# Performance work log

Hardware: AMD Instinct MI355X
Metric: run time of the kernel (lower is better)

The kernel has to match this reference:

```python
import jax, jax.numpy as jnp
import numpy as np

B, N_SRC, N_TGT = 2, 2048, 2048
DIM, HEADS, DIM_HEAD, DIM_ROT = 1024, 16, 64, 32
INNER = HEADS * DIM_HEAD
SCALE = DIM_HEAD ** -0.5


def rotate_every_two(x):
    # (..., d) with d even: pairs (x1, x2) -> (-x2, x1), interleaved
    x1 = x[..., ::2]
    x2 = x[..., 1::2]
    return jnp.stack((-x2, x1), axis=-1).reshape(x.shape)


def setup_inputs() -> dict:
    key = jax.random.key(0)
    ks = jax.random.split(key, 10)
    return {
        "src": jax.random.normal(ks[0], (B, N_SRC, DIM), jnp.float32),
        "sin_src": jax.random.uniform(ks[1], (B, N_SRC, DIM_ROT), jnp.float32, -1.0, 1.0),
        "cos_src": jax.random.uniform(ks[2], (B, N_SRC, DIM_ROT), jnp.float32, -1.0, 1.0),
        "tgt": jax.random.normal(ks[3], (B, N_TGT, DIM), jnp.float32),
        "sin_tgt": jax.random.uniform(ks[4], (B, N_TGT, DIM_ROT), jnp.float32, -1.0, 1.0),
        "cos_tgt": jax.random.uniform(ks[5], (B, N_TGT, DIM_ROT), jnp.float32, -1.0, 1.0),
        "wq": jax.random.normal(ks[6], (DIM, INNER), jnp.float32) / np.sqrt(DIM),
        "wkv": jax.random.normal(ks[7], (DIM, 2 * INNER), jnp.float32) / np.sqrt(DIM),
        "wout": jax.random.normal(ks[8], (INNER, DIM), jnp.float32) / np.sqrt(INNER),
        "bout": jnp.zeros((DIM,), jnp.float32),
    }


def reference(src, sin_src, cos_src, tgt, sin_tgt, cos_tgt, wq, wkv, wout, bout):
    b = src.shape[0]
    q = tgt @ wq                                  # (b, i, inner)
    k, v = jnp.split(src @ wkv, 2, axis=-1)       # (b, j, inner) each

    def split_heads(t):
        return t.reshape(b, t.shape[1], HEADS, DIM_HEAD).transpose(0, 2, 1, 3)

    q, k, v = map(split_heads, (q, k, v))          # (b, h, n, d)

    # rotary on leading DIM_ROT dims; pos embs broadcast across heads
    st, ct = sin_tgt[:, None], cos_tgt[:, None]    # (b, 1, i, dr)
    ss, cs = sin_src[:, None], cos_src[:, None]    # (b, 1, j, dr)
    q_rot, q_pass = q[..., :DIM_ROT], q[..., DIM_ROT:]
    k_rot, k_pass = k[..., :DIM_ROT], k[..., DIM_ROT:]
    q_rot = q_rot * ct + rotate_every_two(q_rot) * st
    k_rot = k_rot * cs + rotate_every_two(k_rot) * ss
    q = jnp.concatenate([q_rot, q_pass], axis=-1)
    k = jnp.concatenate([k_rot, k_pass], axis=-1)

    dots = jnp.einsum('bhid,bhjd->bhij', q, k) * SCALE
    attn = jax.nn.softmax(dots, axis=-1)
    out = jnp.einsum('bhij,bhjd->bhid', attn, v)
    out = out.transpose(0, 2, 1, 3).reshape(b, out.shape[2], INNER)
    return out @ wout + bout, attn
```

## Files before the change

kernel.cpp:

```cpp
#include <hip/hip_runtime.h>
#include <hip/hip_bf16.h>
#include <cstdint>
#include <cstddef>

#define NB 2
#define NSEQ 2048
#define NHEADS 16
#define HD 64
#define DMODEL 1024
#define SCALEF 0.125f

typedef __attribute__((ext_vector_type(4))) float f32x4;
typedef __attribute__((ext_vector_type(8))) short s16x8;

__device__ __forceinline__ unsigned short f2bf(float f) {
  union { float f; unsigned u; } v; v.f = f;
  unsigned u = v.u;
  return (unsigned short)((u + 0x7fffu + ((u >> 16) & 1u)) >> 16);
}
__device__ __forceinline__ float bf2f(unsigned short s) {
  union { unsigned u; float f; } v; v.u = ((unsigned)s) << 16;
  return v.f;
}

__global__ void k_convert2(const float* __restrict__ a, const float* __restrict__ b,
                           unsigned short* __restrict__ oa, unsigned short* __restrict__ ob) {
  int bx = blockIdx.x;
  const float* in = (bx < 4096) ? a : b;
  unsigned short* out = (bx < 4096) ? oa : ob;
  int i = (bx & 4095) * 256 + threadIdx.x;
  float4 v = ((const float4*)in)[i];
  ushort4 o;
  o.x = f2bf(v.x); o.y = f2bf(v.y); o.z = f2bf(v.z); o.w = f2bf(v.w);
  ((ushort4*)out)[i] = o;
}

__global__ void k_transpose_all(const float* __restrict__ wq, unsigned short* __restrict__ wq_t,
                                const float* __restrict__ wkv, unsigned short* __restrict__ wkv_t,
                                const float* __restrict__ wout, unsigned short* __restrict__ wout_t) {
  const int z = blockIdx.z;
  const float* w; unsigned short* wt; int N;
  if (z == 0)      { w = wq;   wt = wq_t;   N = 1024; }
  else if (z == 1) { w = wkv;  wt = wkv_t;  N = 2048; }
  else             { w = wout; wt = wout_t; N = 1024; }
  if (blockIdx.x * 64 >= N) return;
  __shared__ float t[64][65];
  int n0 = blockIdx.x * 64, k0 = blockIdx.y * 64;
  int c = threadIdx.x & 63, rb = threadIdx.x >> 6;
#pragma unroll
  for (int rr = 0; rr < 16; rr++) {
    int k = rb * 16 + rr;
    t[c][k] = w[(size_t)(k0 + k) * N + n0 + c];
  }
  __syncthreads();
#pragma unroll
  for (int rr = 0; rr < 16; rr++) {
    int n = rb * 16 + rr;
    wt[(size_t)(n0 + n) * 1024 + k0 + c] = f2bf(t[n][c]);
  }
}

#define GLD16(gp, lp) __builtin_amdgcn_global_load_lds( \
    (const __attribute__((address_space(1))) unsigned int*)(gp), \
    (__attribute__((address_space(3))) unsigned int*)(lp), 16, 0, 0)

#define GEMM_BODY(A, Bt)                                                        \
  __shared__ unsigned short As[128 * 32];                                       \
  __shared__ unsigned short Bs[128 * 32];                                       \
  const int tid = threadIdx.x;                                                  \
  const int lane = tid & 63, wid = tid >> 6;                                    \
  const int m0 = blockIdx.y * 128, n0 = blockIdx.x * 128;                       \
  const int wr = wid >> 1, wc = wid & 1;                                        \
  const int lr = lane >> 2, l4 = lane & 3;                                      \
  const int lc = lane & 15, lg = lane >> 4;                                     \
  const unsigned short* pa0 = A + (size_t)(m0 + wid * 32 + lr) * 1024 + l4 * 8; \
  const unsigned short* pa1 = pa0 + (size_t)16 * 1024;                          \
  const unsigned short* pb0 = Bt + (size_t)(n0 + wid * 32 + lr) * 1024 + l4 * 8;\
  const unsigned short* pb1 = pb0 + (size_t)16 * 1024;                          \
  f32x4 acc[4][4] = {};                                                         \
  for (int kt = 0; kt < 1024; kt += 32) {                                       \
    GLD16(pa0 + kt, &As[wid * 1024]);                                           \
    GLD16(pa1 + kt, &As[wid * 1024 + 512]);                                     \
    GLD16(pb0 + kt, &Bs[wid * 1024]);                                           \
    GLD16(pb1 + kt, &Bs[wid * 1024 + 512]);                                     \
    __syncthreads();                                                            \
    s16x8 af[4], bfr[4];                                                        \
    _Pragma("unroll")                                                           \
    for (int m = 0; m < 4; m++)                                                 \
      af[m] = *(const s16x8*)&As[(wr * 64 + m * 16 + lc) * 32 + lg * 8];        \
    _Pragma("unroll")                                                           \
    for (int n = 0; n < 4; n++)                                                 \
      bfr[n] = *(const s16x8*)&Bs[(wc * 64 + n * 16 + lc) * 32 + lg * 8];       \
    __builtin_amdgcn_s_setprio(1);                                              \
    _Pragma("unroll")                                                           \
    for (int m = 0; m < 4; m++)                                                 \
      _Pragma("unroll")                                                         \
      for (int n = 0; n < 4; n++)                                               \
        acc[m][n] = __builtin_amdgcn_mfma_f32_16x16x32_bf16(af[m], bfr[n], acc[m][n], 0, 0, 0); \
    __builtin_amdgcn_s_setprio(0);                                              \
    __syncthreads();                                                            \
  }

__global__ __launch_bounds__(256) void k_gemm(const unsigned short* __restrict__ A,
                                              const unsigned short* __restrict__ Bt,
                                              float* __restrict__ C,
                                              const float* __restrict__ bias) {
  GEMM_BODY(A, Bt)
  float bv[4];
#pragma unroll
  for (int n = 0; n < 4; n++) bv[n] = bias[n0 + wc * 64 + n * 16 + lc];
#pragma unroll
  for (int m = 0; m < 4; m++) {
#pragma unroll
    for (int n = 0; n < 4; n++) {
      int col = n0 + wc * 64 + n * 16 + lc;
#pragma unroll
      for (int r = 0; r < 4; r++) {
        int row = m0 + wr * 64 + m * 16 + lg * 4 + r;
        C[(size_t)row * 1024 + col] = acc[m][n][r] + bv[n];
      }
    }
  }
}

__global__ __launch_bounds__(256) void k_gemmq(const unsigned short* __restrict__ A,
                                               const unsigned short* __restrict__ Bt,
                                               const float* __restrict__ sinp,
                                               const float* __restrict__ cosp,
                                               unsigned short* __restrict__ qhb) {
  GEMM_BODY(A, Bt)
#pragma unroll
  for (int m = 0; m < 4; m++) {
#pragma unroll
    for (int n = 0; n < 4; n++) {
      int c = n0 + wc * 64 + n * 16 + lc;
      int h = c >> 6, d = c & 63;
      bool dorope = (d < 32);
#pragma unroll
      for (int r = 0; r < 4; r++) {
        int row = m0 + wr * 64 + m * 16 + lg * 4 + r;
        float x = acc[m][n][r];
        float px = __shfl_xor(x, 1);
        float o = x;
        if (dorope) {
          float s = sinp[(size_t)row * 32 + d];
          float cz = cosp[(size_t)row * 32 + d];
          o = (d & 1) ? (x * cz + px * s) : (x * cz - px * s);
        }
        int b = row >> 11, i = row & 2047;
        qhb[((size_t)(b * NHEADS + h) * NSEQ + i) * HD + d] = f2bf(o);
      }
    }
  }
}

__global__ __launch_bounds__(256) void k_gemmkv(const unsigned short* __restrict__ A,
                                                const unsigned short* __restrict__ Bt,
                                                const float* __restrict__ sinp,
                                                const float* __restrict__ cosp,
                                                unsigned short* __restrict__ khb,
                                                unsigned short* __restrict__ vtb) {
  GEMM_BODY(A, Bt)
#pragma unroll
  for (int m = 0; m < 4; m++) {
#pragma unroll
    for (int n = 0; n < 4; n++) {
      int c = n0 + wc * 64 + n * 16 + lc;
      int d = c & 63;
      if (c < 1024) {
        int h = c >> 6;
        bool dorope = (d < 32);
#pragma unroll
        for (int r = 0; r < 4; r++) {
          int row = m0 + wr * 64 + m * 16 + lg * 4 + r;
          float x = acc[m][n][r];
          float px = __shfl_xor(x, 1);
          float o = x;
          if (dorope) {
            float s = sinp[(size_t)row * 32 + d];
            float cz = cosp[(size_t)row * 32 + d];
            o = (d & 1) ? (x * cz + px * s) : (x * cz - px * s);
          }
          int b = row >> 11, i = row & 2047;
          khb[((size_t)(b * NHEADS + h) * NSEQ + i) * HD + d] = f2bf(o);
        }
      } else {
        int h = (c - 1024) >> 6;
#pragma unroll
        for (int r = 0; r < 4; r++) (void)__shfl_xor(acc[m][n][r], 1);
        ushort4 o;
        o.x = f2bf(acc[m][n][0]); o.y = f2bf(acc[m][n][1]);
        o.z = f2bf(acc[m][n][2]); o.w = f2bf(acc[m][n][3]);
        int row0 = m0 + wr * 64 + m * 16 + lg * 4;
        int b = row0 >> 11, i = row0 & 2047;
        *(ushort4*)&vtb[((size_t)(b * NHEADS + h) * HD + d) * NSEQ + i] = o;
      }
    }
  }
}

#define QBLK 32
#define SROWB 2056
__global__ __launch_bounds__(1024, 4) void k_attn(const unsigned short* __restrict__ qh,
                                                  const unsigned short* __restrict__ kh,
                                                  const unsigned short* __restrict__ vt,
                                                  float* __restrict__ attn_g,
                                                  unsigned short* __restrict__ ctx) {
  __shared__ unsigned short Sbf[QBLK * SROWB];
  __shared__ float wred[16][32];
  __shared__ float invr[32];
  float* part = (float*)Sbf;

  const int tid = threadIdx.x;
  const int lane = tid & 63, wid = tid >> 6;
  const int bid = blockIdx.x;
  const int g = bid & 31, t = bid >> 5;
  const int h = g & 15, b = g >> 4;
  const int i0 = t * QBLK;
  const int lc = lane & 15, lg = lane >> 4;
  const int wcb = wid * 128;

  const unsigned short* qb = qh + ((size_t)(b * NHEADS + h) * NSEQ + i0) * HD;
  const unsigned short* kb = kh + (size_t)(b * NHEADS + h) * NSEQ * HD;
  const unsigned short* vb = vt + (size_t)(b * NHEADS + h) * HD * NSEQ;

  s16x8 aq[2][2];
#pragma unroll
  for (int rg = 0; rg < 2; rg++) {
    aq[rg][0] = *(const s16x8*)&qb[(rg * 16 + lc) * HD + lg * 8];
    aq[rg][1] = *(const s16x8*)&qb[(rg * 16 + lc) * HD + 32 + lg * 8];
  }
  float psum[2][4] = {};
  const unsigned short* krow = kb + (size_t)(wcb + lc) * HD + lg * 8;
  s16x8 kp[2][2];
  kp[0][0] = *(const s16x8*)&krow[0];
  kp[0][1] = *(const s16x8*)&krow[32];
#pragma unroll
  for (int jf = 0; jf < 8; jf++) {
    if (jf < 7) {
      kp[(jf + 1) & 1][0] = *(const s16x8*)&krow[(size_t)((jf + 1) * 16) * HD];
      kp[(jf + 1) & 1][1] = *(const s16x8*)&krow[(size_t)((jf + 1) * 16) * HD + 32];
    }
    int j = wcb + jf * 16;
#pragma unroll
    for (int rg = 0; rg < 2; rg++) {
      f32x4 acc = {};
      acc = __builtin_amdgcn_mfma_f32_16x16x32_bf16(aq[rg][0], kp[jf & 1][0], acc, 0, 0, 0);
      acc = __builtin_amdgcn_mfma_f32_16x16x32_bf16(aq[rg][1], kp[jf & 1][1], acc, 0, 0, 0);
#pragma unroll
      for (int r = 0; r < 4; r++) {
        float e = __expf(acc[r] * SCALEF);
        psum[rg][r] += e;
        Sbf[(size_t)(rg * 16 + lg * 4 + r) * SROWB + j + lc] = f2bf(e);
      }
    }
  }
#pragma unroll
  for (int off = 1; off <= 8; off <<= 1)
#pragma unroll
    for (int rg = 0; rg < 2; rg++)
#pragma unroll
      for (int r = 0; r < 4; r++) psum[rg][r] += __shfl_xor(psum[rg][r], off);
  if (lc == 0) {
#pragma unroll
    for (int rg = 0; rg < 2; rg++)
#pragma unroll
      for (int r = 0; r < 4; r++) wred[wid][rg * 16 + lg * 4 + r] = psum[rg][r];
  }
  __syncthreads();
  if (tid < 32) {
    float tot = 0.f;
#pragma unroll
    for (int w = 0; w < 16; w++) tot += wred[w][tid];
    invr[tid] = 1.0f / tot;
  }
  __syncthreads();

  const int srow = tid >> 5;
  const int scc = (tid & 31) * 8;
  const float sinv = invr[srow];
  float* arow = attn_g + ((size_t)(b * NHEADS + h) * NSEQ + i0 + srow) * NSEQ + scc;

  f32x4 accd[2][4] = {};
  const unsigned short* vrow = vb + (size_t)lc * NSEQ + wcb + lg * 8;
  s16x8 vp[2][4];
#pragma unroll
  for (int f = 0; f < 4; f++)
    vp[0][f] = *(const s16x8*)&vrow[(size_t)(f * 16) * NSEQ];
#pragma unroll
  for (int jj = 0; jj < 4; jj++) {
    if (jj < 3) {
#pragma unroll
      for (int f = 0; f < 4; f++)
        vp[(jj + 1) & 1][f] = *(const s16x8*)&vrow[(size_t)(f * 16) * NSEQ + (jj + 1) * 32];
    }
    int jb = wcb + jj * 32;
    s16x8 af0 = *(const s16x8*)&Sbf[(size_t)lc * SROWB + jb + lg * 8];
    __builtin_amdgcn_s_setprio(1);
#pragma unroll
    for (int f = 0; f < 4; f++)
      accd[0][f] = __builtin_amdgcn_mfma_f32_16x16x32_bf16(af0, vp[jj & 1][f], accd[0][f], 0, 0, 0);
    __builtin_amdgcn_s_setprio(0);
    s16x8 af1 = *(const s16x8*)&Sbf[(size_t)(16 + lc) * SROWB + jb + lg * 8];
    __builtin_amdgcn_s_setprio(1);
#pragma unroll
    for (int f = 0; f < 4; f++)
      accd[1][f] = __builtin_amdgcn_mfma_f32_16x16x32_bf16(af1, vp[jj & 1][f], accd[1][f], 0, 0, 0);
    __builtin_amdgcn_s_setprio(0);
#pragma unroll
    for (int kk = 0; kk < 2; kk++) {
      int k = jj * 2 + kk;
      s16x8 ev = *(const s16x8*)&Sbf[(size_t)srow * SROWB + scc + k * 256];
      f32x4 f0, f1;
      f0[0] = bf2f((unsigned short)ev[0]) * sinv;
      f0[1] = bf2f((unsigned short)ev[1]) * sinv;
      f0[2] = bf2f((unsigned short)ev[2]) * sinv;
      f0[3] = bf2f((unsigned short)ev[3]) * sinv;
      f1[0] = bf2f((unsigned short)ev[4]) * sinv;
      f1[1] = bf2f((unsigned short)ev[5]) * sinv;
      f1[2] = bf2f((unsigned short)ev[6]) * sinv;
      f1[3] = bf2f((unsigned short)ev[7]) * sinv;
      *(f32x4*)&arow[k * 256] = f0;
      *(f32x4*)&arow[k * 256 + 4] = f1;
    }
  }
  __syncthreads();

  if (wid < 8) {
#pragma unroll
    for (int rg = 0; rg < 2; rg++)
#pragma unroll
      for (int f = 0; f < 4; f++)
#pragma unroll
        for (int r = 0; r < 4; r++)
          part[((size_t)wid * 32 + rg * 16 + lg * 4 + r) * 65 + f * 16 + lc] = accd[rg][f][r];
  }
  __syncthreads();
  if (wid >= 8) {
#pragma unroll
    for (int rg = 0; rg < 2; rg++)
#pragma unroll
      for (int f = 0; f < 4; f++)
#pragma unroll
        for (int r = 0; r < 4; r++)
          part[((size_t)(wid - 8) * 32 + rg * 16 + lg * 4 + r) * 65 + f * 16 + lc] += accd[rg][f][r];
  }
  __syncthreads();

  {
    const int oi = tid >> 5;
    const int d0 = (tid & 31) * 2;
    float s0 = 0.f, s1 = 0.f;
#pragma unroll
    for (int p = 0; p < 8; p++) {
      s0 += part[((size_t)p * 32 + oi) * 65 + d0];
      s1 += part[((size_t)p * 32 + oi) * 65 + d0 + 1];
    }
    float iv = invr[oi];
    ushort2 o;
    o.x = f2bf(s0 * iv);
    o.y = f2bf(s1 * iv);
    *(ushort2*)&ctx[(size_t)(b * NSEQ + i0 + oi) * DMODEL + h * HD + d0] = o;
  }
}

extern "C" void kernel_launch(void* const* d_in, const int* in_sizes, int n_in,
                              void* d_out, int out_size, void* d_ws, size_t ws_size,
                              hipStream_t stream) {
  const float* src     = (const float*)d_in[0];
  const float* sin_src = (const float*)d_in[1];
  const float* cos_src = (const float*)d_in[2];
  const float* tgt     = (const float*)d_in[3];
  const float* sin_tgt = (const float*)d_in[4];
  const float* cos_tgt = (const float*)d_in[5];
  const float* wq      = (const float*)d_in[6];
  const float* wkv     = (const float*)d_in[7];
  const float* wout    = (const float*)d_in[8];
  const float* bout    = (const float*)d_in[9];

  if (ws_size < (size_t)109051904) return;

  uint8_t* w = (uint8_t*)d_ws;
  unsigned short* tgt_bf = (unsigned short*)(w + 0);
  unsigned short* src_bf = (unsigned short*)(w + 8388608);
  unsigned short* wq_t   = (unsigned short*)(w + 16777216);
  unsigned short* wkv_t  = (unsigned short*)(w + 18874368);
  unsigned short* wout_t = (unsigned short*)(w + 23068672);
  unsigned short* qhb    = (unsigned short*)(w + 75497472);
  unsigned short* khb    = (unsigned short*)(w + 83886080);
  unsigned short* vtb    = (unsigned short*)(w + 92274688);
  unsigned short* ctx    = (unsigned short*)(w + 100663296);

  float* out_p  = (float*)d_out;
  float* attn_p = out_p + (size_t)NB * NSEQ * DMODEL;

  k_convert2<<<8192, 256, 0, stream>>>(tgt, src, tgt_bf, src_bf);
  k_transpose_all<<<dim3(32, 16, 3), 256, 0, stream>>>(wq, wq_t, wkv, wkv_t, wout, wout_t);

  k_gemmq <<<dim3(8, 32),  256, 0, stream>>>(tgt_bf, wq_t,  sin_tgt, cos_tgt, qhb);
  k_gemmkv<<<dim3(16, 32), 256, 0, stream>>>(src_bf, wkv_t, sin_src, cos_src, khb, vtb);

  k_attn<<<2048, 1024, 0, stream>>>(qhb, khb, vtb, attn_p, ctx);

  k_gemm<<<dim3(8, 32), 256, 0, stream>>>(ctx, wout_t, out_p, bout);
}
```

Before: 337.8 us.

## Halve attention query block to 16 rows with 512-thread blocks

The attention kernel now processes 16 query rows per block with 8 waves, each covering 256 keys, instead of 32 rows with 16 waves covering 128 keys. Grid doubles to 4096 blocks and LDS per block halves, which lets more blocks reside per CU and shortens each block's serial phases. In exchange, every K/V element is reloaded twice as often across blocks, and each wave now runs longer loops with fewer MFMAs per loaded K/V fragment.

```diff
diff --git a/kernel.cpp b/kernel.cpp
--- a/kernel.cpp
+++ b/kernel.cpp
@@ -199,16 +199,16 @@
   }
 }
 
-#define QBLK 32
+#define QBLK 16
 #define SROWB 2056
-__global__ __launch_bounds__(1024, 4) void k_attn(const unsigned short* __restrict__ qh,
-                                                  const unsigned short* __restrict__ kh,
-                                                  const unsigned short* __restrict__ vt,
-                                                  float* __restrict__ attn_g,
-                                                  unsigned short* __restrict__ ctx) {
+__global__ __launch_bounds__(512, 4) void k_attn(const unsigned short* __restrict__ qh,
+                                                 const unsigned short* __restrict__ kh,
+                                                 const unsigned short* __restrict__ vt,
+                                                 float* __restrict__ attn_g,
+                                                 unsigned short* __restrict__ ctx) {
   __shared__ unsigned short Sbf[QBLK * SROWB];
-  __shared__ float wred[16][32];
-  __shared__ float invr[32];
+  __shared__ float wred[8][16];
+  __shared__ float invr[16];
   float* part = (float*)Sbf;
 
   const int tid = threadIdx.x;
@@ -218,60 +218,49 @@
   const int h = g & 15, b = g >> 4;
   const int i0 = t * QBLK;
   const int lc = lane & 15, lg = lane >> 4;
-  const int wcb = wid * 128;
+  const int wcb = wid * 256;
 
   const unsigned short* qb = qh + ((size_t)(b * NHEADS + h) * NSEQ + i0) * HD;
   const unsigned short* kb = kh + (size_t)(b * NHEADS + h) * NSEQ * HD;
   const unsigned short* vb = vt + (size_t)(b * NHEADS + h) * HD * NSEQ;
 
-  s16x8 aq[2][2];
-#pragma unroll
-  for (int rg = 0; rg < 2; rg++) {
-    aq[rg][0] = *(const s16x8*)&qb[(rg * 16 + lc) * HD + lg * 8];
-    aq[rg][1] = *(const s16x8*)&qb[(rg * 16 + lc) * HD + 32 + lg * 8];
-  }
-  float psum[2][4] = {};
+  s16x8 aq0 = *(const s16x8*)&qb[lc * HD + lg * 8];
+  s16x8 aq1 = *(const s16x8*)&qb[lc * HD + 32 + lg * 8];
+  float psum[4] = {};
   const unsigned short* krow = kb + (size_t)(wcb + lc) * HD + lg * 8;
   s16x8 kp[2][2];
   kp[0][0] = *(const s16x8*)&krow[0];
   kp[0][1] = *(const s16x8*)&krow[32];
 #pragma unroll
-  for (int jf = 0; jf < 8; jf++) {
-    if (jf < 7) {
+  for (int jf = 0; jf < 16; jf++) {
+    if (jf < 15) {
       kp[(jf + 1) & 1][0] = *(const s16x8*)&krow[(size_t)((jf + 1) * 16) * HD];
       kp[(jf + 1) & 1][1] = *(const s16x8*)&krow[(size_t)((jf + 1) * 16) * HD + 32];
     }
     int j = wcb + jf * 16;
-#pragma unroll
-    for (int rg = 0; rg < 2; rg++) {
-      f32x4 acc = {};
-      acc = __builtin_amdgcn_mfma_f32_16x16x32_bf16(aq[rg][0], kp[jf & 1][0], acc, 0, 0, 0);
-      acc = __builtin_amdgcn_mfma_f32_16x16x32_bf16(aq[rg][1], kp[jf & 1][1], acc, 0, 0, 0);
-#pragma unroll
-      for (int r = 0; r < 4; r++) {
-        float e = __expf(acc[r] * SCALEF);
-        psum[rg][r] += e;
-        Sbf[(size_t)(rg * 16 + lg * 4 + r) * SROWB + j + lc] = f2bf(e);
-      }
+    f32x4 acc = {};
+    acc = __builtin_amdgcn_mfma_f32_16x16x32_bf16(aq0, kp[jf & 1][0], acc, 0, 0, 0);
+    acc = __builtin_amdgcn_mfma_f32_16x16x32_bf16(aq1, kp[jf & 1][1], acc, 0, 0, 0);
+#pragma unroll
+    for (int r = 0; r < 4; r++) {
+      float e = __expf(acc[r] * SCALEF);
+      psum[r] += e;
+      Sbf[(size_t)(lg * 4 + r) * SROWB + j + lc] = f2bf(e);
     }
   }
 #pragma unroll
   for (int off = 1; off <= 8; off <<= 1)
 #pragma unroll
-    for (int rg = 0; rg < 2; rg++)
-#pragma unroll
-      for (int r = 0; r < 4; r++) psum[rg][r] += __shfl_xor(psum[rg][r], off);
+    for (int r = 0; r < 4; r++) psum[r] += __shfl_xor(psum[r], off);
   if (lc == 0) {
 #pragma unroll
-    for (int rg = 0; rg < 2; rg++)
-#pragma unroll
-      for (int r = 0; r < 4; r++) wred[wid][rg * 16 + lg * 4 + r] = psum[rg][r];
-  }
-  __syncthreads();
-  if (tid < 32) {
+    for (int r = 0; r < 4; r++) wred[wid][lg * 4 + r] = psum[r];
+  }
+  __syncthreads();
+  if (tid < 16) {
     float tot = 0.f;
 #pragma unroll
-    for (int w = 0; w < 16; w++) tot += wred[w][tid];
+    for (int w = 0; w < 8; w++) tot += wred[w][tid];
     invr[tid] = 1.0f / tot;
   }
   __syncthreads();
@@ -281,36 +270,28 @@
   const float sinv = invr[srow];
   float* arow = attn_g + ((size_t)(b * NHEADS + h) * NSEQ + i0 + srow) * NSEQ + scc;
 
-  f32x4 accd[2][4] = {};
+  f32x4 accd[4] = {};
   const unsigned short* vrow = vb + (size_t)lc * NSEQ + wcb + lg * 8;
   s16x8 vp[2][4];
 #pragma unroll
   for (int f = 0; f < 4; f++)
     vp[0][f] = *(const s16x8*)&vrow[(size_t)(f * 16) * NSEQ];
 #pragma unroll
-  for (int jj = 0; jj < 4; jj++) {
-    if (jj < 3) {
+  for (int jj = 0; jj < 8; jj++) {
+    if (jj < 7) {
 #pragma unroll
       for (int f = 0; f < 4; f++)
         vp[(jj + 1) & 1][f] = *(const s16x8*)&vrow[(size_t)(f * 16) * NSEQ + (jj + 1) * 32];
     }
     int jb = wcb + jj * 32;
-    s16x8 af0 = *(const s16x8*)&Sbf[(size_t)lc * SROWB + jb + lg * 8];
+    s16x8 af = *(const s16x8*)&Sbf[(size_t)lc * SROWB + jb + lg * 8];
     __builtin_amdgcn_s_setprio(1);
 #pragma unroll
     for (int f = 0; f < 4; f++)
-      accd[0][f] = __builtin_amdgcn_mfma_f32_16x16x32_bf16(af0, vp[jj & 1][f], accd[0][f], 0, 0, 0);
+      accd[f] = __builtin_amdgcn_mfma_f32_16x16x32_bf16(af, vp[jj & 1][f], accd[f], 0, 0, 0);
     __builtin_amdgcn_s_setprio(0);
-    s16x8 af1 = *(const s16x8*)&Sbf[(size_t)(16 + lc) * SROWB + jb + lg * 8];
-    __builtin_amdgcn_s_setprio(1);
-#pragma unroll
-    for (int f = 0; f < 4; f++)
-      accd[1][f] = __builtin_amdgcn_mfma_f32_16x16x32_bf16(af1, vp[jj & 1][f], accd[1][f], 0, 0, 0);
-    __builtin_amdgcn_s_setprio(0);
-#pragma unroll
-    for (int kk = 0; kk < 2; kk++) {
-      int k = jj * 2 + kk;
-      s16x8 ev = *(const s16x8*)&Sbf[(size_t)srow * SROWB + scc + k * 256];
+    {
+      s16x8 ev = *(const s16x8*)&Sbf[(size_t)srow * SROWB + scc + jj * 256];
       f32x4 f0, f1;
       f0[0] = bf2f((unsigned short)ev[0]) * sinv;
       f0[1] = bf2f((unsigned short)ev[1]) * sinv;
@@ -320,30 +301,26 @@
       f1[1] = bf2f((unsigned short)ev[5]) * sinv;
       f1[2] = bf2f((unsigned short)ev[6]) * sinv;
       f1[3] = bf2f((unsigned short)ev[7]) * sinv;
-      *(f32x4*)&arow[k * 256] = f0;
-      *(f32x4*)&arow[k * 256 + 4] = f1;
-    }
-  }
-  __syncthreads();
-
-  if (wid < 8) {
-#pragma unroll
-    for (int rg = 0; rg < 2; rg++)
-#pragma unroll
-      for (int f = 0; f < 4; f++)
-#pragma unroll
-        for (int r = 0; r < 4; r++)
-          part[((size_t)wid * 32 + rg * 16 + lg * 4 + r) * 65 + f * 16 + lc] = accd[rg][f][r];
-  }
-  __syncthreads();
-  if (wid >= 8) {
-#pragma unroll
-    for (int rg = 0; rg < 2; rg++)
-#pragma unroll
-      for (int f = 0; f < 4; f++)
-#pragma unroll
-        for (int r = 0; r < 4; r++)
-          part[((size_t)(wid - 8) * 32 + rg * 16 + lg * 4 + r) * 65 + f * 16 + lc] += accd[rg][f][r];
+      *(f32x4*)&arow[jj * 256] = f0;
+      *(f32x4*)&arow[jj * 256 + 4] = f1;
+    }
+  }
+  __syncthreads();
+
+  if (wid < 4) {
+#pragma unroll
+    for (int f = 0; f < 4; f++)
+#pragma unroll
+      for (int r = 0; r < 4; r++)
+        part[((size_t)wid * 16 + lg * 4 + r) * 65 + f * 16 + lc] = accd[f][r];
+  }
+  __syncthreads();
+  if (wid >= 4) {
+#pragma unroll
+    for (int f = 0; f < 4; f++)
+#pragma unroll
+      for (int r = 0; r < 4; r++)
+        part[((size_t)(wid - 4) * 16 + lg * 4 + r) * 65 + f * 16 + lc] += accd[f][r];
   }
   __syncthreads();
 
@@ -352,9 +329,9 @@
     const int d0 = (tid & 31) * 2;
     float s0 = 0.f, s1 = 0.f;
 #pragma unroll
-    for (int p = 0; p < 8; p++) {
-      s0 += part[((size_t)p * 32 + oi) * 65 + d0];
-      s1 += part[((size_t)p * 32 + oi) * 65 + d0 + 1];
+    for (int p = 0; p < 4; p++) {
+      s0 += part[((size_t)p * 16 + oi) * 65 + d0];
+      s1 += part[((size_t)p * 16 + oi) * 65 + d0 + 1];
     }
     float iv = invr[oi];
     ushort2 o;
@@ -400,7 +377,7 @@
   k_gemmq <<<dim3(8, 32),  256, 0, stream>>>(tgt_bf, wq_t,  sin_tgt, cos_tgt, qhb);
   k_gemmkv<<<dim3(16, 32), 256, 0, stream>>>(src_bf, wkv_t, sin_src, cos_src, khb, vtb);
 
-  k_attn<<<2048, 1024, 0, stream>>>(qhb, khb, vtb, attn_p, ctx);
+  k_attn<<<4096, 512, 0, stream>>>(qhb, khb, vtb, attn_p, ctx);
 
   k_gemm<<<dim3(8, 32), 256, 0, stream>>>(ctx, wout_t, out_p, bout);
 }
```

Measured after the change: 406.5 us. 1.2x slower.
